# Kernel optimization log

Measured on AMD Instinct MI355X. Metric: run time of the kernel, lower is better.

The kernel has to match this reference:

```python
import jax, jax.numpy as jnp
import numpy as np

D_MODEL = 1024
N_HEADS = 16
D_K = D_MODEL // N_HEADS  # 64
D_FF = int(8 * D_MODEL / 3)  # 2730
THETA = 10000.0
MAX_SEQ_LEN = 2048
BATCH = 2
SEQ = 2048
EPS = 1e-5


def setup_inputs() -> dict:
    key = jax.random.key(0)
    ks = jax.random.split(key, 10)

    def lin(k, d_out, d_in):
        sigma = np.sqrt(2.0 / (d_out + d_in))
        w = jax.random.truncated_normal(k, -3.0, 3.0, (d_out, d_in), dtype=jnp.float32)
        return w * sigma

    x = jax.random.normal(ks[0], (BATCH, SEQ, D_MODEL), dtype=jnp.float32)
    token_positions = jnp.tile(jnp.arange(SEQ, dtype=jnp.int32)[None, :], (BATCH, 1))
    return {
        "x": x,
        "token_positions": token_positions,
        "WQ": lin(ks[1], D_MODEL, D_MODEL),
        "WK": lin(ks[2], D_MODEL, D_MODEL),
        "WV": lin(ks[3], D_MODEL, D_MODEL),
        "WO": lin(ks[4], D_MODEL, D_MODEL),
        "W1": lin(ks[5], D_FF, D_MODEL),
        "W2": lin(ks[6], D_MODEL, D_FF),
        "W3": lin(ks[7], D_FF, D_MODEL),
        "g1": jnp.ones((D_MODEL,), dtype=jnp.float32),
        "g2": jnp.ones((D_MODEL,), dtype=jnp.float32),
    }


def _rmsnorm(x, g):
    xf = x.astype(jnp.float32)
    inv = jax.lax.rsqrt(jnp.mean(xf * xf, axis=-1, keepdims=True) + EPS)
    return (xf * inv * g).astype(x.dtype)


def _rope(x, pos):
    # x: [b, h, t, d_k]; pos: [b, t] int. Pairs are consecutive (x0,x1).
    half = D_K // 2
    inv_freq = THETA ** (-(2.0 * jnp.arange(1, half + 1, dtype=jnp.float32) - 2.0) / D_K)
    ang = pos.astype(jnp.float32)[..., None] * inv_freq  # [b, t, half]
    cos = jnp.cos(ang)[:, None, :, :]  # [b, 1, t, half]
    sin = jnp.sin(ang)[:, None, :, :]
    xr = x.reshape(*x.shape[:-1], half, 2)
    x0, x1 = xr[..., 0], xr[..., 1]
    out = jnp.stack([cos * x0 - sin * x1, sin * x0 + cos * x1], axis=-1)
    return out.reshape(x.shape)


def reference(x, token_positions, WQ, WK, WV, WO, W1, W2, W3, g1, g2):
    b, t, _ = x.shape
    # --- attention sublayer (pre-norm) ---
    h = _rmsnorm(x, g1)
    q = jnp.einsum('btd,ed->bte', h, WQ).reshape(b, t, N_HEADS, D_K).transpose(0, 2, 1, 3)
    k = jnp.einsum('btd,ed->bte', h, WK).reshape(b, t, N_HEADS, D_K).transpose(0, 2, 1, 3)
    v = jnp.einsum('btd,ed->bte', h, WV).reshape(b, t, N_HEADS, D_K).transpose(0, 2, 1, 3)
    q = _rope(q, token_positions)
    k = _rope(k, token_positions)
    scores = jnp.einsum('bhqd,bhkd->bhqk', q, k) * (D_K ** -0.5)
    causal = jnp.tril(jnp.ones((t, t), dtype=bool))
    scores = jnp.where(causal, scores, -jnp.inf)
    attn = jax.nn.softmax(scores, axis=-1)
    o = jnp.einsum('bhqk,bhkd->bhqd', attn, v)
    o = o.transpose(0, 2, 1, 3).reshape(b, t, D_MODEL)
    o = jnp.einsum('btd,ed->bte', o, WO)
    x = x + o
    # --- SwiGLU FFN sublayer (pre-norm) ---
    h = _rmsnorm(x, g2)
    u = jnp.einsum('btd,fd->btf', h, W1)
    g = jnp.einsum('btd,fd->btf', h, W3)
    ff = jnp.einsum('btf,df->btd', (u * jax.nn.sigmoid(u)) * g, W2)
    return x + ff
```

## Files before the change

### kernel.cpp

```cpp
#include <hip/hip_runtime.h>
#include <cstdint>

#define BT_ROWS 4096
#define DM      1024
#define DFF     2730
#define DFFP    2816
#define TSEQ    2048

typedef float  f32x4  __attribute__((ext_vector_type(4)));
typedef __bf16 bf16x8 __attribute__((ext_vector_type(8)));

typedef __attribute__((address_space(1))) const unsigned int as1_uint;
typedef __attribute__((address_space(3))) unsigned int       as3_uint;

__device__ __forceinline__ unsigned short f2bf(float f) {
  union { float f; unsigned int u; } v; v.f = f;
  unsigned int u = v.u;
  return (unsigned short)((u + 0x7fffu + ((u >> 16) & 1u)) >> 16);
}
__device__ __forceinline__ float bf2f(unsigned int b) {
  union { unsigned int u; float f; } v; v.u = b << 16;
  return v.f;
}

__device__ __forceinline__ void async_cp16(const void* g, void* l) {
  __builtin_amdgcn_global_load_lds((as1_uint*)(uintptr_t)g, (as3_uint*)(uintptr_t)l, 16, 0, 0);
}

#define PREP_BLOCKS 12672
__global__ void prep_kernel(const float* __restrict__ WQ, const float* __restrict__ WK,
                            const float* __restrict__ WV, const float* __restrict__ WOp,
                            const float* __restrict__ W1, const float* __restrict__ W3,
                            const float* __restrict__ W2, const int* __restrict__ pos,
                            unsigned short* __restrict__ Wqkv, unsigned short* __restrict__ Wo,
                            unsigned short* __restrict__ W13i, unsigned short* __restrict__ W2p,
                            float2* __restrict__ cs,
                            const float* __restrict__ x, const float* __restrict__ g1,
                            unsigned short* __restrict__ hbuf) {
  if (blockIdx.x >= PREP_BLOCKS) {
    const int row = blockIdx.x - PREP_BLOCKS, tid = threadIdx.x;
    const float4 xv = reinterpret_cast<const float4*>(x + (long)row * DM)[tid];
    float ss = xv.x * xv.x + xv.y * xv.y + xv.z * xv.z + xv.w * xv.w;
#pragma unroll
    for (int o = 32; o > 0; o >>= 1) ss += __shfl_xor(ss, o);
    __shared__ float wsum[4];
    if ((tid & 63) == 0) wsum[tid >> 6] = ss;
    __syncthreads();
    const float inv = rsqrtf((wsum[0] + wsum[1] + wsum[2] + wsum[3]) * (1.f / DM) + 1e-5f);
    const float4 gv = reinterpret_cast<const float4*>(g1)[tid];
    ushort4 o4;
    o4.x = f2bf(xv.x * inv * gv.x);
    o4.y = f2bf(xv.y * inv * gv.y);
    o4.z = f2bf(xv.z * inv * gv.z);
    o4.w = f2bf(xv.w * inv * gv.w);
    reinterpret_cast<ushort4*>(hbuf + (long)row * DM)[tid] = o4;
    return;
  }
  long grp = (long)blockIdx.x * 256 + threadIdx.x;
  if (grp < 1048576) {
    const int j = (int)(grp >> 18);
    const long t = (grp & 262143L) * 4;
    const float* s = (j == 0) ? WQ : (j == 1) ? WK : (j == 2) ? WV : WOp;
    unsigned short* d = (j < 3) ? (Wqkv + (size_t)j * 1048576) : Wo;
    const float4 v = *reinterpret_cast<const float4*>(s + t);
    *reinterpret_cast<ushort4*>(d + t) =
        make_ushort4(f2bf(v.x), f2bf(v.y), f2bf(v.z), f2bf(v.w));
    return;
  }
  grp -= 1048576;
  if (grp < 1441792) {
    const int half = (int)(grp / 720896);
    const long t = (grp % 720896) * 4;
    const int r = (int)(t >> 10), c = (int)(t & 1023);
    ushort4 o = make_ushort4(0, 0, 0, 0);
    if (r < DFF) {
      const float4 v = *reinterpret_cast<const float4*>(((half ? W3 : W1) + (long)r * 1024 + c));
      o = make_ushort4(f2bf(v.x), f2bf(v.y), f2bf(v.z), f2bf(v.w));
    }
    *reinterpret_cast<ushort4*>(W13i + ((long)2 * r + half) * 1024 + c) = o;
    return;
  }
  grp -= 1441792;
  if (grp < 720896) {
    const long t = grp * 4;
    const int r = (int)(t / DFFP), c = (int)(t % DFFP);
    const float* src = W2 + (long)r * DFF + c;
    ushort4 o;
    o.x = (c     < DFF) ? f2bf(src[0]) : 0;
    o.y = (c + 1 < DFF) ? f2bf(src[1]) : 0;
    o.z = (c + 2 < DFF) ? f2bf(src[2]) : 0;
    o.w = (c + 3 < DFF) ? f2bf(src[3]) : 0;
    *reinterpret_cast<ushort4*>(W2p + t) = o;
    return;
  }
  grp -= 720896;
  if (grp < 32768) {
    const long i0 = grp * 4;
    const int r = (int)(i0 >> 5);
    const float p = (float)pos[r];
#pragma unroll
    for (int j = 0; j < 4; ++j) {
      const int i = (int)((i0 + j) & 31);
      const float f = powf(10000.f, -(float)(2 * i) * (1.f / 64.f));
      float sv, cv;
      sincosf(p * f, &sv, &cv);
      cs[i0 + j] = make_float2(cv, sv);
    }
  }
}

__global__ void rmsnorm_bf16_kernel(const unsigned short* __restrict__ x, const float* __restrict__ g,
                                    unsigned short* __restrict__ out) {
  const int row = blockIdx.x, tid = threadIdx.x;
  const ushort4 xu = reinterpret_cast<const ushort4*>(x + (long)row * DM)[tid];
  const float x0 = bf2f(xu.x), x1 = bf2f(xu.y), x2 = bf2f(xu.z), x3 = bf2f(xu.w);
  float ss = x0 * x0 + x1 * x1 + x2 * x2 + x3 * x3;
#pragma unroll
  for (int o = 32; o > 0; o >>= 1) ss += __shfl_xor(ss, o);
  __shared__ float wsum[4];
  if ((tid & 63) == 0) wsum[tid >> 6] = ss;
  __syncthreads();
  const float inv = rsqrtf((wsum[0] + wsum[1] + wsum[2] + wsum[3]) * (1.f / DM) + 1e-5f);
  const float4 gv = reinterpret_cast<const float4*>(g)[tid];
  ushort4 o4;
  o4.x = f2bf(x0 * inv * gv.x);
  o4.y = f2bf(x1 * inv * gv.y);
  o4.z = f2bf(x2 * inv * gv.z);
  o4.w = f2bf(x3 * inv * gv.w);
  reinterpret_cast<ushort4*>(out + (long)row * DM)[tid] = o4;
}

template <int EPI, int BN, int DB>
__global__ __launch_bounds__(256) void gemm_bt(
    const unsigned short* __restrict__ A, const unsigned short* __restrict__ B,
    void* __restrict__ C, const float* __restrict__ resid,
    const float2* __restrict__ CS,
    int M, int N, int K, int ldc) {
  constexpr int WNF = BN / 32;
  __shared__ unsigned short As[(DB + 1) * 128 * 64];
  __shared__ unsigned short Bs[(DB + 1) * BN * 64];
  const int tid = threadIdx.x;
  const int wid = tid >> 6;
  const int lane = tid & 63;
  const int nwg = gridDim.x * gridDim.y;
  int flat = blockIdx.y * gridDim.x + blockIdx.x;
  flat = (flat & 7) * (nwg >> 3) + (flat >> 3);
  const int bx = flat / gridDim.y;
  const int by = flat % gridDim.y;
  const long rowBase = (long)by * 128;
  const long colBase = (long)bx * BN;
  const int wm = (wid >> 1) * 64;
  const int wn = (wid & 1) * (BN / 2);
  const int srow = wid * 8 + (lane >> 3);
  const int sc   = lane & 7;
  const int cs   = (sc ^ (srow & 7)) * 8;
  const int fr = lane & 15;
  const int fg = lane >> 4;

  const f32x4 z4 = {0.f, 0.f, 0.f, 0.f};
  f32x4 acc[4][WNF];
#pragma unroll
  for (int m = 0; m < 4; ++m)
#pragma unroll
    for (int n = 0; n < WNF; ++n) acc[m][n] = z4;

  auto stage = [&](int buf, int kt) {
    const long kOff = (long)kt * 64 + cs;
    char* AsB = (char*)As + buf * 16384;
    char* BsB = (char*)Bs + buf * (BN * 128);
#pragma unroll
    for (int i = 0; i < 4; ++i)
      async_cp16(A + (rowBase + i * 32 + srow) * K + kOff, AsB + i * 4096 + wid * 1024);
#pragma unroll
    for (int i = 0; i < WNF; ++i)
      async_cp16(B + (colBase + i * 32 + srow) * K + kOff, BsB + i * 4096 + wid * 1024);
  };

  auto compute = [&](int buf) {
    const char* AsB = (const char*)As + buf * 16384;
    const char* BsB = (const char*)Bs + buf * (BN * 128);
#pragma unroll
    for (int kk = 0; kk < 2; ++kk) {
      bf16x8 af[4], bfr[WNF];
#pragma unroll
      for (int m = 0; m < 4; ++m)
        af[m] = *(const bf16x8*)(AsB + (wm + m * 16 + fr) * 128 + (((kk * 4 + fg) ^ (fr & 7)) * 16));
#pragma unroll
      for (int n = 0; n < WNF; ++n)
        bfr[n] = *(const bf16x8*)(BsB + (wn + n * 16 + fr) * 128 + (((kk * 4 + fg) ^ (fr & 7)) * 16));
#pragma unroll
      for (int m = 0; m < 4; ++m)
#pragma unroll
        for (int n = 0; n < WNF; ++n)
          acc[m][n] = __builtin_amdgcn_mfma_f32_16x16x32_bf16(af[m], bfr[n], acc[m][n], 0, 0, 0);
    }
  };

  const int nkt = K >> 6;
  if (DB) {
    stage(0, 0);
    __syncthreads();
    for (int kt = 0; kt < nkt; ++kt) {
      if (kt + 1 < nkt) stage((kt + 1) & 1, kt + 1);
      compute(kt & 1);
      __syncthreads();
    }
  } else {
    for (int kt = 0; kt < nkt; ++kt) {
      if (kt) __syncthreads();
      stage(0, kt);
      __syncthreads();
      compute(0);
    }
  }

  const int erow = fg * 4;
  if (EPI == 0) {
    unsigned short* Cp = (unsigned short*)C;
#pragma unroll
    for (int m = 0; m < 4; ++m) {
      const long r0 = rowBase + wm + m * 16 + erow;
#pragma unroll
      for (int n = 0; n < WNF; ++n) {
        const long col = colBase + wn + n * 16 + fr;
#pragma unroll
        for (int r = 0; r < 4; ++r) Cp[(r0 + r) * ldc + col] = f2bf(acc[m][n][r]);
      }
    }
  } else if (EPI == 5) {
    unsigned short* Cp = (unsigned short*)C;
#pragma unroll
    for (int m = 0; m < 4; ++m) {
      const long r0 = rowBase + wm + m * 16 + erow;
#pragma unroll
      for (int n = 0; n < WNF; ++n) {
        const long col = colBase + wn + n * 16 + fr;
#pragma unroll
        for (int r = 0; r < 4; ++r) {
          const long o = (r0 + r) * ldc + col;
          Cp[o] = f2bf(acc[m][n][r] + resid[o]);
        }
      }
    }
  } else if (EPI == 6) {
    float* Cf = (float*)C;
    const unsigned short* Rb = (const unsigned short*)(const void*)resid;
#pragma unroll
    for (int m = 0; m < 4; ++m) {
      const long r0 = rowBase + wm + m * 16 + erow;
#pragma unroll
      for (int n = 0; n < WNF; ++n) {
        const long col = colBase + wn + n * 16 + fr;
#pragma unroll
        for (int r = 0; r < 4; ++r) {
          const long o = (r0 + r) * ldc + col;
          Cf[o] = acc[m][n][r] + bf2f(Rb[o]);
        }
      }
    }
  } else if (EPI == 3) {
    unsigned short* Cp = (unsigned short*)C;
    const int even = !(fr & 1);
#pragma unroll
    for (int m = 0; m < 4; ++m) {
      const long r0 = rowBase + wm + m * 16 + erow;
#pragma unroll
      for (int n = 0; n < WNF; ++n) {
        const long col = colBase + wn + n * 16 + fr;
        const long fcol = col >> 1;
#pragma unroll
        for (int r = 0; r < 4; ++r) {
          const float own = acc[m][n][r];
          const float oth = __shfl_xor(own, 1);
          if (even) {
            const float s = own * oth / (1.f + __expf(-own));
            Cp[(r0 + r) * ldc + fcol] = f2bf(s);
          }
        }
      }
    }
  } else {
    unsigned short* Cp = (unsigned short*)C;
    const int even = !(fr & 1);
#pragma unroll
    for (int m = 0; m < 4; ++m) {
      const long r0 = rowBase + wm + m * 16 + erow;
#pragma unroll
      for (int n = 0; n < WNF; ++n) {
        const long col = colBase + wn + n * 16 + fr;
        const int i = (int)((col & 63) >> 1);
#pragma unroll
        for (int r = 0; r < 4; ++r) {
          const float own = acc[m][n][r];
          const float oth = __shfl_xor(own, 1);
          const float2 cv = CS[(r0 + r) * 32 + i];
          const float v = even ? (cv.x * own - cv.y * oth) : (cv.y * oth + cv.x * own);
          Cp[(r0 + r) * ldc + col] = f2bf(v);
        }
      }
    }
  }
}

#define KSTR 72
__global__ __launch_bounds__(256) void attn_kernel(
    const unsigned short* __restrict__ QK, const unsigned short* __restrict__ Vt,
    unsigned short* __restrict__ O) {
  __shared__ unsigned short Ks[2][64 * KSTR];
  const int bh = blockIdx.x;
  const int b = bh >> 4, h = bh & 15;
  const int tid = threadIdx.x;
  const int wid = tid >> 6, lane = tid & 63;
  const int fr = lane & 15, g = lane >> 4;
  const long rowb = (long)b * TSEQ;
  const int hoff = h * 64;
  const float C2 = 0.18033688011112042f;

  const int ki = tid >> 3;
  const int kcol = (tid & 7) * 8;
  const int kgrow = 8 * ((ki & 15) >> 2) + (ki & 3) + ((ki >> 4) << 2);

  const unsigned short* Kg = QK + rowb * 2048 + 1024 + hoff;
  const unsigned short* Vrow = Vt + (long)(hoff + fr) * 4096 + rowb + g * 8;
  const f32x4 z4 = {0.f, 0.f, 0.f, 0.f};
  bf16x8 onesv;
#pragma unroll
  for (int j = 0; j < 8; ++j) onesv[j] = (__bf16)1.0f;

#pragma unroll
  for (int phase = 0; phase < 2; ++phase) {
    const int qblk = phase ? (31 - blockIdx.y) : blockIdx.y;
    const int qbase = qblk * 64 + wid * 16;
    const int qg = qbase + fr;
    const int nkt = qblk + 1;

    const unsigned short* qrow = QK + (rowb + qbase + fr) * 2048 + hoff + g * 8;
    const bf16x8 qb0 = *reinterpret_cast<const bf16x8*>(qrow);
    const bf16x8 qb1 = *reinterpret_cast<const bf16x8*>(qrow + 32);

    f32x4 acc[4];
#pragma unroll
    for (int d = 0; d < 4; ++d) acc[d] = z4;
    f32x4 accL = z4;
    float mrun = -1e30f;

    uint4 kr0 = *reinterpret_cast<const uint4*>(Kg + (long)kgrow * 2048 + kcol);
    uint4 kr1 = *reinterpret_cast<const uint4*>(Kg + (long)(32 + kgrow) * 2048 + kcol);

    __syncthreads();

    for (int kt = 0; kt < nkt; ++kt) {
      unsigned short* Kb = Ks[kt & 1];
      *reinterpret_cast<uint4*>(&Kb[ki * KSTR + kcol]) = kr0;
      *reinterpret_cast<uint4*>(&Kb[(32 + ki) * KSTR + kcol]) = kr1;
      __syncthreads();
      const int kbase = kt * 64;
      if (kt + 1 < nkt) {
        kr0 = *reinterpret_cast<const uint4*>(Kg + (long)(kbase + 64 + kgrow) * 2048 + kcol);
        kr1 = *reinterpret_cast<const uint4*>(Kg + (long)(kbase + 96 + kgrow) * 2048 + kcol);
      }
      bf16x8 vf[4][2];
#pragma unroll
      for (int db = 0; db < 4; ++db)
#pragma unroll
        for (int ks = 0; ks < 2; ++ks)
          vf[db][ks] = *reinterpret_cast<const bf16x8*>(Vrow + (size_t)db * 16 * 4096 + kbase + ks * 32);

      f32x4 s1[2], s2[2];
#pragma unroll
      for (int ks = 0; ks < 2; ++ks) {
        const unsigned short* ra = &Kb[(ks * 32 + fr) * KSTR];
        const unsigned short* rc = &Kb[(ks * 32 + 16 + fr) * KSTR];
        f32x4 t1 = z4, t2 = z4;
        t1 = __builtin_amdgcn_mfma_f32_16x16x32_bf16(*reinterpret_cast<const bf16x8*>(ra + g * 8), qb0, t1, 0, 0, 0);
        t1 = __builtin_amdgcn_mfma_f32_16x16x32_bf16(*reinterpret_cast<const bf16x8*>(ra + 32 + g * 8), qb1, t1, 0, 0, 0);
        t2 = __builtin_amdgcn_mfma_f32_16x16x32_bf16(*reinterpret_cast<const bf16x8*>(rc + g * 8), qb0, t2, 0, 0, 0);
        t2 = __builtin_amdgcn_mfma_f32_16x16x32_bf16(*reinterpret_cast<const bf16x8*>(rc + 32 + g * 8), qb1, t2, 0, 0, 0);
        s1[ks] = t1; s2[ks] = t2;
      }

      float sc[16];
      if (kt + 1 < nkt) {
#pragma unroll
        for (int ks = 0; ks < 2; ++ks)
#pragma unroll
          for (int j = 0; j < 4; ++j) {
            sc[ks * 8 + j] = s1[ks][j];
            sc[ks * 8 + 4 + j] = s2[ks][j];
          }
      } else {
        const int kb8 = kbase + 8 * g;
#pragma unroll
        for (int ks = 0; ks < 2; ++ks)
#pragma unroll
          for (int j = 0; j < 4; ++j) {
            sc[ks * 8 + j]     = (kb8 + ks * 32 + j     <= qg) ? s1[ks][j] : -1e30f;
            sc[ks * 8 + 4 + j] = (kb8 + ks * 32 + 4 + j <= qg) ? s2[ks][j] : -1e30f;
          }
      }
      const float t0 = fmaxf(fmaxf(sc[0], sc[1]), sc[2]);
      const float t1 = fmaxf(fmaxf(sc[3], sc[4]), sc[5]);
      const float t2 = fmaxf(fmaxf(sc[6], sc[7]), sc[8]);
      const float t3 = fmaxf(fmaxf(sc[9], sc[10]), sc[11]);
      const float t4 = fmaxf(fmaxf(sc[12], sc[13]), sc[14]);
      float tmax = fmaxf(fmaxf(fmaxf(t0, t1), t2), fmaxf(fmaxf(t3, t4), sc[15]));
      const float p1 = __shfl_xor(tmax, 16);
      const float p2 = __shfl_xor(tmax, 32);
      const float p3 = __shfl_xor(tmax, 48);
      tmax = fmaxf(fmaxf(tmax, p1), fmaxf(p2, p3));
      if (__any(tmax > mrun)) {
        const float mnew = fmaxf(mrun, tmax);
        const float alpha = exp2f((mrun - mnew) * C2);
#pragma unroll
        for (int db = 0; db < 4; ++db)
#pragma unroll
          for (int r = 0; r < 4; ++r) acc[db][r] *= alpha;
#pragma unroll
        for (int r = 0; r < 4; ++r) accL[r] *= alpha;
        mrun = mnew;
      }
      const float m2 = mrun * C2;
      bf16x8 pbv[2];
#pragma unroll
      for (int ks = 0; ks < 2; ++ks)
#pragma unroll
        for (int j = 0; j < 8; ++j)
          pbv[ks][j] = (__bf16)exp2f(fmaf(sc[ks * 8 + j], C2, -m2));

#pragma unroll
      for (int db = 0; db < 4; ++db) {
        acc[db] = __builtin_amdgcn_mfma_f32_16x16x32_bf16(vf[db][0], pbv[0], acc[db], 0, 0, 0);
        acc[db] = __builtin_amdgcn_mfma_f32_16x16x32_bf16(vf[db][1], pbv[1], acc[db], 0, 0, 0);
      }
      accL = __builtin_amdgcn_mfma_f32_16x16x32_bf16(onesv, pbv[0], accL, 0, 0, 0);
      accL = __builtin_amdgcn_mfma_f32_16x16x32_bf16(onesv, pbv[1], accL, 0, 0, 0);
    }

    const float inv = 1.f / accL[0];
    unsigned short* orow = O + (rowb + qbase + fr) * DM + hoff;
#pragma unroll
    for (int db = 0; db < 4; ++db) {
      uint2 pk;
      pk.x = (unsigned int)f2bf(acc[db][0] * inv) | ((unsigned int)f2bf(acc[db][1] * inv) << 16);
      pk.y = (unsigned int)f2bf(acc[db][2] * inv) | ((unsigned int)f2bf(acc[db][3] * inv) << 16);
      *reinterpret_cast<uint2*>(orow + db * 16 + g * 4) = pk;
    }
  }
}

static constexpr size_t OFF_WQKV = 0;
static constexpr size_t OFF_WO   = 6291456;
static constexpr size_t OFF_W13  = 8388608;
static constexpr size_t OFF_W2   = 19922944;
static constexpr size_t OFF_H    = 25690112;
static constexpr size_t OFF_X2   = 34078720;
static constexpr size_t OFF_CS   = 50855936;
static constexpr size_t OFF_QK   = 51904512;
static constexpr size_t OFF_VT   = 68681728;
static constexpr size_t OFF_HO   = 77070336;

extern "C" void kernel_launch(void* const* d_in, const int* in_sizes, int n_in,
                              void* d_out, int out_size, void* d_ws, size_t ws_size,
                              hipStream_t stream) {
  const float* x  = (const float*)d_in[0];
  const int* tpos = (const int*)d_in[1];
  const float* WQ = (const float*)d_in[2];
  const float* WK = (const float*)d_in[3];
  const float* WV = (const float*)d_in[4];
  const float* WO = (const float*)d_in[5];
  const float* W1 = (const float*)d_in[6];
  const float* W2 = (const float*)d_in[7];
  const float* W3 = (const float*)d_in[8];
  const float* g1 = (const float*)d_in[9];
  const float* g2 = (const float*)d_in[10];
  float* out = (float*)d_out;

  char* ws = (char*)d_ws;
  unsigned short* Wqkv = (unsigned short*)(ws + OFF_WQKV);
  unsigned short* Wo   = (unsigned short*)(ws + OFF_WO);
  unsigned short* W13i = (unsigned short*)(ws + OFF_W13);
  unsigned short* W2p  = (unsigned short*)(ws + OFF_W2);
  unsigned short* hbuf = (unsigned short*)(ws + OFF_H);
  unsigned short* x2b  = (unsigned short*)(ws + OFF_X2);
  float2* cs           = (float2*)(ws + OFF_CS);
  unsigned short* QKb  = (unsigned short*)(ws + OFF_QK);
  unsigned short* Sbuf = (unsigned short*)(ws + OFF_QK);
  unsigned short* Vtb  = (unsigned short*)(ws + OFF_VT);
  unsigned short* Ho   = (unsigned short*)(ws + OFF_HO);

  prep_kernel<<<PREP_BLOCKS + BT_ROWS, 256, 0, stream>>>(
      WQ, WK, WV, WO, W1, W3, W2, tpos, Wqkv, Wo, W13i, W2p, cs, x, g1, hbuf);

  gemm_bt<4, 128, 1><<<dim3(16, 32), 256, 0, stream>>>(hbuf, Wqkv, QKb, nullptr, cs, BT_ROWS, 2048, 1024, 2048);
  gemm_bt<0, 64, 1><<<dim3(64, 8), 256, 0, stream>>>(Wqkv + 2048 * 1024, hbuf, Vtb, nullptr, nullptr, 1024, BT_ROWS, 1024, BT_ROWS);
  attn_kernel<<<dim3(32, 16), 256, 0, stream>>>(QKb, Vtb, Ho);
  gemm_bt<5, 64, 1><<<dim3(16, 32), 256, 0, stream>>>(Ho, Wo, x2b, x, nullptr, BT_ROWS, 1024, 1024, 1024);

  rmsnorm_bf16_kernel<<<BT_ROWS, 256, 0, stream>>>(x2b, g2, hbuf);
  gemm_bt<3, 128, 0><<<dim3(44, 32), 256, 0, stream>>>(hbuf, W13i, Sbuf, nullptr, nullptr, BT_ROWS, 2 * DFFP, 1024, DFFP);
  gemm_bt<6, 64, 1><<<dim3(16, 32), 256, 0, stream>>>(Sbuf, W2p, out, (const float*)(const void*)x2b, nullptr, BT_ROWS, 1024, DFFP, 1024);
}
```

Measured before the change: 242.0 us.

## Use dedicated 256x256-tile 512-thread GEMM for fused W1/W3 SwiGLU projection

```diff
diff --git a/kernel.cpp b/kernel.cpp
--- a/kernel.cpp
+++ b/kernel.cpp
@@ -258,27 +258,6 @@
         }
       }
     }
-  } else if (EPI == 3) {
-    unsigned short* Cp = (unsigned short*)C;
-    const int even = !(fr & 1);
-#pragma unroll
-    for (int m = 0; m < 4; ++m) {
-      const long r0 = rowBase + wm + m * 16 + erow;
-#pragma unroll
-      for (int n = 0; n < WNF; ++n) {
-        const long col = colBase + wn + n * 16 + fr;
-        const long fcol = col >> 1;
-#pragma unroll
-        for (int r = 0; r < 4; ++r) {
-          const float own = acc[m][n][r];
-          const float oth = __shfl_xor(own, 1);
-          if (even) {
-            const float s = own * oth / (1.f + __expf(-own));
-            Cp[(r0 + r) * ldc + fcol] = f2bf(s);
-          }
-        }
-      }
-    }
   } else {
     unsigned short* Cp = (unsigned short*)C;
     const int even = !(fr & 1);
@@ -296,6 +275,101 @@
           const float2 cv = CS[(r0 + r) * 32 + i];
           const float v = even ? (cv.x * own - cv.y * oth) : (cv.y * oth + cv.x * own);
           Cp[(r0 + r) * ldc + col] = f2bf(v);
+        }
+      }
+    }
+  }
+}
+
+__global__ __launch_bounds__(512) void gemm256_swiglu(
+    const unsigned short* __restrict__ A, const unsigned short* __restrict__ B,
+    unsigned short* __restrict__ C, int M, int N, int K, int ldc) {
+  __shared__ unsigned short LDS[2][2][256 * 64];
+  const int tid = threadIdx.x;
+  const int wid = tid >> 6;
+  const int lane = tid & 63;
+  const int wr = wid >> 2;
+  const int wc = wid & 3;
+  const int nwg = gridDim.x * gridDim.y;
+  int flat = blockIdx.y * gridDim.x + blockIdx.x;
+  flat = (flat & 7) * (nwg >> 3) + (flat >> 3);
+  const int bx = flat / gridDim.y;
+  const int by = flat % gridDim.y;
+  const long rowBase = (long)by * 256;
+  const long colBase = (long)bx * 256;
+  const int srow = tid >> 3;
+  const int sc = tid & 7;
+  const int fr = lane & 15, fg = lane >> 4;
+
+  const f32x4 z4 = {0.f, 0.f, 0.f, 0.f};
+  f32x4 acc[8][4];
+#pragma unroll
+  for (int m = 0; m < 8; ++m)
+#pragma unroll
+    for (int n = 0; n < 4; ++n) acc[m][n] = z4;
+
+  auto stage = [&](int buf, int kt) {
+    const long kOff = (long)kt * 64;
+    char* Ab = (char*)LDS[buf][0];
+    char* Bb = (char*)LDS[buf][1];
+#pragma unroll
+    for (int i = 0; i < 4; ++i) {
+      const int row = i * 64 + srow;
+      const long csrc = kOff + (long)((sc ^ (row & 7)) * 8);
+      async_cp16(A + (rowBase + row) * K + csrc, Ab + i * 8192 + wid * 1024);
+      async_cp16(B + (colBase + row) * K + csrc, Bb + i * 8192 + wid * 1024);
+    }
+  };
+
+  auto compute = [&](int buf) {
+    const char* Ab = (const char*)LDS[buf][0];
+    const char* Bb = (const char*)LDS[buf][1];
+    bf16x8 bfr[4][2];
+#pragma unroll
+    for (int n = 0; n < 4; ++n) {
+      const int row = wc * 64 + n * 16 + fr;
+#pragma unroll
+      for (int kk = 0; kk < 2; ++kk)
+        bfr[n][kk] = *(const bf16x8*)(Bb + row * 128 + (((kk * 4 + fg) ^ (fr & 7)) * 16));
+    }
+#pragma unroll
+    for (int m = 0; m < 8; ++m) {
+      const int row = wr * 128 + m * 16 + fr;
+      const bf16x8 af0 = *(const bf16x8*)(Ab + row * 128 + (((fg) ^ (fr & 7)) * 16));
+      const bf16x8 af1 = *(const bf16x8*)(Ab + row * 128 + (((4 + fg) ^ (fr & 7)) * 16));
+#pragma unroll
+      for (int n = 0; n < 4; ++n) {
+        acc[m][n] = __builtin_amdgcn_mfma_f32_16x16x32_bf16(af0, bfr[n][0], acc[m][n], 0, 0, 0);
+        acc[m][n] = __builtin_amdgcn_mfma_f32_16x16x32_bf16(af1, bfr[n][1], acc[m][n], 0, 0, 0);
+      }
+    }
+  };
+
+  const int nkt = K >> 6;
+  stage(0, 0);
+  __syncthreads();
+  for (int kt = 0; kt < nkt; ++kt) {
+    if (kt + 1 < nkt) stage((kt + 1) & 1, kt + 1);
+    compute(kt & 1);
+    __syncthreads();
+  }
+
+  const int erow = fg * 4;
+  const int even = !(fr & 1);
+#pragma unroll
+  for (int m = 0; m < 8; ++m) {
+    const long r0 = rowBase + wr * 128 + m * 16 + erow;
+#pragma unroll
+    for (int n = 0; n < 4; ++n) {
+      const long col = colBase + wc * 64 + n * 16 + fr;
+      const long fcol = col >> 1;
+#pragma unroll
+      for (int r = 0; r < 4; ++r) {
+        const float own = acc[m][n][r];
+        const float oth = __shfl_xor(own, 1);
+        if (even) {
+          const float s = own * oth / (1.f + __expf(-own));
+          C[(r0 + r) * ldc + fcol] = f2bf(s);
         }
       }
     }
@@ -497,6 +571,6 @@
   gemm_bt<5, 64, 1><<<dim3(16, 32), 256, 0, stream>>>(Ho, Wo, x2b, x, nullptr, BT_ROWS, 1024, 1024, 1024);
 
   rmsnorm_bf16_kernel<<<BT_ROWS, 256, 0, stream>>>(x2b, g2, hbuf);
-  gemm_bt<3, 128, 0><<<dim3(44, 32), 256, 0, stream>>>(hbuf, W13i, Sbuf, nullptr, nullptr, BT_ROWS, 2 * DFFP, 1024, DFFP);
+  gemm256_swiglu<<<dim3(22, 16), 512, 0, stream>>>(hbuf, W13i, Sbuf, BT_ROWS, 2 * DFFP, 1024, DFFP);
   gemm_bt<6, 64, 1><<<dim3(16, 32), 256, 0, stream>>>(Sbuf, W2p, out, (const float*)(const void*)x2b, nullptr, BT_ROWS, 1024, DFFP, 1024);
 }
```

Result: slower. 257.5 us (+6.4%).

## Replace W1/W3 SwiGLU GEMM with 256x256 tiled, 8-wave pipelined kernel

Applied to the files above, without the earlier changes.

```diff
diff --git a/kernel.cpp b/kernel.cpp
--- a/kernel.cpp
+++ b/kernel.cpp
@@ -258,27 +258,6 @@
         }
       }
     }
-  } else if (EPI == 3) {
-    unsigned short* Cp = (unsigned short*)C;
-    const int even = !(fr & 1);
-#pragma unroll
-    for (int m = 0; m < 4; ++m) {
-      const long r0 = rowBase + wm + m * 16 + erow;
-#pragma unroll
-      for (int n = 0; n < WNF; ++n) {
-        const long col = colBase + wn + n * 16 + fr;
-        const long fcol = col >> 1;
-#pragma unroll
-        for (int r = 0; r < 4; ++r) {
-          const float own = acc[m][n][r];
-          const float oth = __shfl_xor(own, 1);
-          if (even) {
-            const float s = own * oth / (1.f + __expf(-own));
-            Cp[(r0 + r) * ldc + fcol] = f2bf(s);
-          }
-        }
-      }
-    }
   } else {
     unsigned short* Cp = (unsigned short*)C;
     const int even = !(fr & 1);
@@ -300,6 +279,137 @@
       }
     }
   }
+}
+
+#define PH256(BUF, MH, NH, DOSTAGE, SBUF, SKT, SMAT, SHALF)                     \
+  {                                                                             \
+    const char* Ab = (const char*)Al[BUF];                                      \
+    const char* Bb = (const char*)Bl[BUF];                                      \
+    bf16x8 af[4][2], bfv[2][2];                                                 \
+    _Pragma("unroll")                                                           \
+    for (int m = 0; m < 4; ++m) {                                               \
+      const int arow = (MH) * 128 + m * 32 + wr * 16 + fr;                      \
+      _Pragma("unroll")                                                         \
+      for (int kk = 0; kk < 2; ++kk)                                            \
+        af[m][kk] = *(const bf16x8*)(Ab + arow * 128 + (((kk * 4 + fg) ^ (fr & 7)) * 16)); \
+    }                                                                           \
+    _Pragma("unroll")                                                           \
+    for (int n = 0; n < 2; ++n) {                                               \
+      const int brow = (NH) * 128 + n * 64 + wc * 16 + fr;                      \
+      _Pragma("unroll")                                                         \
+      for (int kk = 0; kk < 2; ++kk)                                            \
+        bfv[n][kk] = *(const bf16x8*)(Bb + brow * 128 + (((kk * 4 + fg) ^ (fr & 7)) * 16)); \
+    }                                                                           \
+    if (DOSTAGE) stageHT(SBUF, SKT, SMAT, SHALF);                               \
+    __builtin_amdgcn_sched_barrier(0);                                          \
+    __builtin_amdgcn_s_barrier();                                               \
+    __builtin_amdgcn_sched_barrier(0);                                          \
+    __builtin_amdgcn_s_setprio(1);                                              \
+    _Pragma("unroll")                                                           \
+    for (int m = 0; m < 4; ++m)                                                 \
+      _Pragma("unroll")                                                         \
+      for (int n = 0; n < 2; ++n) {                                             \
+        acc[(MH) * 4 + m][(NH) * 2 + n] = __builtin_amdgcn_mfma_f32_16x16x32_bf16( \
+            af[m][0], bfv[n][0], acc[(MH) * 4 + m][(NH) * 2 + n], 0, 0, 0);     \
+        acc[(MH) * 4 + m][(NH) * 2 + n] = __builtin_amdgcn_mfma_f32_16x16x32_bf16( \
+            af[m][1], bfv[n][1], acc[(MH) * 4 + m][(NH) * 2 + n], 0, 0, 0);     \
+      }                                                                         \
+    __builtin_amdgcn_s_setprio(0);                                              \
+    __builtin_amdgcn_sched_barrier(0);                                          \
+  }
+
+__global__ __launch_bounds__(512) void gemm256p_swiglu(
+    const unsigned short* __restrict__ A, const unsigned short* __restrict__ B,
+    unsigned short* __restrict__ C, int M, int N, int K, int ldc) {
+  __shared__ unsigned short Al[2][256 * 64];
+  __shared__ unsigned short Bl[2][256 * 64];
+  const int tid = threadIdx.x;
+  const int wid = tid >> 6, lane = tid & 63;
+  const int wr = wid >> 2, wc = wid & 3;
+  const int fr = lane & 15, fg = lane >> 4;
+  const int nwg = gridDim.x * gridDim.y;
+  int flat = blockIdx.y * gridDim.x + blockIdx.x;
+  flat = (flat & 7) * (nwg >> 3) + (flat >> 3);
+  const int bx = flat / gridDim.y;
+  const int by = flat % gridDim.y;
+  const long rowBase = (long)by * 256;
+  const long colBase = (long)bx * 256;
+  const int srow_l = tid >> 3;
+  const int sch = tid & 7;
+
+  const f32x4 z4 = {0.f, 0.f, 0.f, 0.f};
+  f32x4 acc[8][4];
+#pragma unroll
+  for (int m = 0; m < 8; ++m)
+#pragma unroll
+    for (int n = 0; n < 4; ++n) acc[m][n] = z4;
+
+  auto stageHT = [&](int buf, int kt, int mat, int half) {
+    const unsigned short* G = mat ? B : A;
+    const long base = mat ? colBase : rowBase;
+    char* L = (char*)(mat ? Bl[buf] : Al[buf]) + half * 16384;
+    const long kOff = (long)kt * 64;
+#pragma unroll
+    for (int i = 0; i < 2; ++i) {
+      const int row = half * 128 + i * 64 + srow_l;
+      async_cp16(G + (base + row) * K + kOff + ((sch ^ (row & 7)) * 8),
+                 L + i * 8192 + wid * 1024);
+    }
+  };
+
+  const int nkt = K >> 6;
+  stageHT(0, 0, 0, 0); stageHT(0, 0, 1, 0);
+  stageHT(0, 0, 0, 1); stageHT(0, 0, 1, 1);
+  stageHT(1, 1, 0, 0); stageHT(1, 1, 1, 0);
+  asm volatile("s_waitcnt vmcnt(4)" ::: "memory");
+  __builtin_amdgcn_sched_barrier(0);
+  __builtin_amdgcn_s_barrier();
+  __builtin_amdgcn_sched_barrier(0);
+
+  for (int kt = 0; kt < nkt; ++kt) {
+    const int buf = kt & 1, nbuf = buf ^ 1;
+    const bool s1 = (kt + 1 < nkt), s2 = (kt + 2 < nkt);
+    PH256(buf, 0, 0, s1, nbuf, kt + 1, 0, 1);
+    __builtin_amdgcn_s_barrier();
+    __builtin_amdgcn_sched_barrier(0);
+    PH256(buf, 0, 1, s1, nbuf, kt + 1, 1, 1);
+    __builtin_amdgcn_s_barrier();
+    __builtin_amdgcn_sched_barrier(0);
+    PH256(buf, 1, 0, s2, buf, kt + 2, 0, 0);
+    __builtin_amdgcn_s_barrier();
+    __builtin_amdgcn_sched_barrier(0);
+    PH256(buf, 1, 1, s2, buf, kt + 2, 1, 0);
+    if (s2) asm volatile("s_waitcnt vmcnt(4)" ::: "memory");
+    else    asm volatile("s_waitcnt vmcnt(0)" ::: "memory");
+    __builtin_amdgcn_sched_barrier(0);
+    __builtin_amdgcn_s_barrier();
+    __builtin_amdgcn_sched_barrier(0);
+  }
+
+  const int erow = fg * 4;
+  const int even = !(fr & 1);
+#pragma unroll
+  for (int mh = 0; mh < 2; ++mh)
+#pragma unroll
+    for (int m = 0; m < 4; ++m) {
+      const long r0 = rowBase + mh * 128 + m * 32 + wr * 16 + erow;
+#pragma unroll
+      for (int nh = 0; nh < 2; ++nh)
+#pragma unroll
+        for (int n = 0; n < 2; ++n) {
+          const long col = colBase + nh * 128 + n * 64 + wc * 16 + fr;
+          const long fcol = col >> 1;
+#pragma unroll
+          for (int r = 0; r < 4; ++r) {
+            const float own = acc[mh * 4 + m][nh * 2 + n][r];
+            const float oth = __shfl_xor(own, 1);
+            if (even) {
+              const float s = own * oth / (1.f + __expf(-own));
+              C[(r0 + r) * ldc + fcol] = f2bf(s);
+            }
+          }
+        }
+    }
 }
 
 #define KSTR 72
@@ -497,6 +607,6 @@
   gemm_bt<5, 64, 1><<<dim3(16, 32), 256, 0, stream>>>(Ho, Wo, x2b, x, nullptr, BT_ROWS, 1024, 1024, 1024);
 
   rmsnorm_bf16_kernel<<<BT_ROWS, 256, 0, stream>>>(x2b, g2, hbuf);
-  gemm_bt<3, 128, 0><<<dim3(44, 32), 256, 0, stream>>>(hbuf, W13i, Sbuf, nullptr, nullptr, BT_ROWS, 2 * DFFP, 1024, DFFP);
+  gemm256p_swiglu<<<dim3(22, 16), 512, 0, stream>>>(hbuf, W13i, Sbuf, BT_ROWS, 2 * DFFP, 1024, DFFP);
   gemm_bt<6, 64, 1><<<dim3(16, 32), 256, 0, stream>>>(Sbuf, W2p, out, (const float*)(const void*)x2b, nullptr, BT_ROWS, 1024, DFFP, 1024);
 }
```

Result: slower. 270.6 us (+11.8%).
